# Performance work log

Hardware: AMD Instinct MI355X
Metric: run time of the kernel (lower is better)

## Reference

```python
import jax, jax.numpy as jnp
import numpy as np

DX, DY, MR, MBAR, NT, B, GOUT = 16, 8, 64, 256, 9, 4, 64
HX, EX, HRNN, HB = 1024, 512, 512, 2048
BB_IN = 1 + EX + HRNN


def setup_inputs() -> dict:
    key = jax.random.key(0)
    ks = jax.random.split(key, 12)
    total = (NT - 1) * MBAR + 1  # 2049 hidden-process time points
    X = jax.random.randint(ks[0], (B, total, DX), 0, 50).astype(jnp.float32)  # molecule counts
    Y = jax.random.normal(ks[1], (B, NT, DY), dtype=jnp.float32)
    # R: cumulative integrated reaction rates (non-decreasing in time)
    R = jnp.cumsum(jax.random.uniform(ks[2], (B, total, MR), dtype=jnp.float32) * 0.01, axis=1)
    stoich = (jax.random.randint(ks[3], (DX, MR), 0, 3) - 1).astype(jnp.float32)  # entries in {-1,0,1}
    times_t = jnp.linspace(0.0, 8.0, NT).astype(jnp.float32)
    times_tau = jnp.linspace(0.0, 1.0, MBAR).astype(jnp.float32)
    sc = lambda k, sh: jax.random.normal(k, sh, dtype=jnp.float32) * np.float32(1.0 / np.sqrt(sh[0]))
    Wx1, bx1 = sc(ks[4], (DX, HX)), jnp.zeros(HX, jnp.float32)
    Wx2, bx2 = sc(ks[5], (HX, EX)), jnp.zeros(EX, jnp.float32)
    Wih = sc(ks[6], (DY, HRNN))
    Whh = sc(ks[7], (HRNN, HRNN))
    bh = jnp.zeros(HRNN, jnp.float32)
    Wb1, bb1 = sc(ks[8], (BB_IN, HB)), jnp.zeros(HB, jnp.float32)
    Wb2, bb2 = sc(ks[9], (HB, GOUT)), jnp.zeros(GOUT, jnp.float32)
    return dict(X=X, Y=Y, R=R, stoich=stoich, times_t=times_t, times_tau=times_tau,
                Wx1=Wx1, bx1=bx1, Wx2=Wx2, bx2=bx2, Wih=Wih, Whh=Whh, bh=bh,
                Wb1=Wb1, bb1=bb1, Wb2=Wb2, bb2=bb2, k=1, k_prime=1, q=0, q_prime=1)


def reference(X, Y, R, stoich, times_t, times_tau,
              Wx1, bx1, Wx2, bx2, Wih, Whh, bh, Wb1, bb1, Wb2, bb2,
              k, k_prime, q, q_prime):
    """stochastic_integral_vectorized: gather displaced states, run the
    martingale network forward on base and displaced states, masked
    accumulation weighted by rate increments. Returns [GOUT]."""
    m_bar = times_tau.shape[0]
    base = k_prime * m_bar

    # --- Y encoder (Elman RNN over the observation slice, final hidden state) ---
    Yslice = Y[q, k + 1:, :]                       # [T_rem, DY]
    def rnn_step(h, y):
        return jnp.tanh(y @ Wih + h @ Whh + bh), None
    eY, _ = jax.lax.scan(rnn_step, jnp.zeros(Whh.shape[0], X.dtype), Yslice)  # [HRNN]

    # --- batched martingale forward: t [N], Xb [N, DX] -> [N, GOUT] ---
    def batched_forward(t, Xb):
        eX = jnp.tanh(Xb @ Wx1 + bx1) @ Wx2 + bx2          # [N, EX]
        eYb = jnp.broadcast_to(eY, (Xb.shape[0], eY.shape[0]))
        inp = jnp.concatenate([t[:, None], eX, eYb], axis=1)  # [N, 1+EX+HRNN]
        return jnp.tanh(inp @ Wb1 + bb1) @ Wb2 + bb2       # [N, GOUT]

    Xbase = X[q_prime, base:base + m_bar, :]               # [M_bar, DX]
    t = times_t[k] + times_tau                              # [M_bar]
    nn = batched_forward(t, Xbase)                          # [M_bar, GOUT]

    mr = stoich.shape[1]
    X_disp = Xbase[None, :, :] + stoich.T[:, None, :]       # [MR, M_bar, DX]
    valid = jnp.all(X_disp >= 0, axis=-1)                   # [MR, M_bar]
    nn_disp = batched_forward(jnp.tile(t, mr),
                              X_disp.reshape(mr * m_bar, -1)).reshape(mr, m_bar, -1)

    R_delta = R[q_prime, base + 1:base + m_bar + 1, :] - R[q_prime, base:base + m_bar, :]  # [M_bar, MR]
    si = jnp.einsum('jmg,mj,jm->g', nn_disp - nn[None], R_delta, valid.astype(nn.dtype))
    return si
```

## Files before the change

### kernel.cpp

```cpp
#include <hip/hip_runtime.h>
#include <math.h>

#define DXc   16
#define MRc   64
#define MBARc 256
#define NTc   9
#define DYc   8
#define HXc   1024
#define EXc   512
#define HRc   512
#define HBc   2048
#define GOUTc 64
#define TOTc  2049

using bf16x8 = __attribute__((ext_vector_type(8))) short;
using f32x4  = __attribute__((ext_vector_type(4))) float;

typedef unsigned int u32;
typedef u32 __attribute__((address_space(1))) gbl_u32;
typedef u32 __attribute__((address_space(3))) lds_u32;

__device__ __forceinline__ float fast_tanh(float x){
    float e = __expf(2.0f * x);
    return 1.0f - 2.0f / (e + 1.0f);
}

__device__ __forceinline__ short f2bf(float f){
    unsigned u = __builtin_bit_cast(unsigned, f);
    u = (u + 0x7FFFu + ((u >> 16) & 1u)) >> 16;
    return (short)u;
}

__device__ __forceinline__ void gld_lds16(const short* g, short* l){
    __builtin_amdgcn_global_load_lds((const gbl_u32*)g, (lds_u32*)l, 16, 0, 0);
}

__global__ void prep_kernel(const float* __restrict__ stoich, const float* __restrict__ Wx1,
                            const float* __restrict__ Wx2, const float* __restrict__ Wb1,
                            const float* __restrict__ X, const float* __restrict__ R,
                            const float* __restrict__ bx1, const float* __restrict__ bx2,
                            const int* kpptr, const int* qpptr,
                            float* __restrict__ SW, short* __restrict__ Wx2a,
                            short* __restrict__ Wb1p, float* __restrict__ XW,
                            float* __restrict__ T1, float* __restrict__ wrow,
                            float* __restrict__ hb0, float* __restrict__ dacc,
                            float* __restrict__ outz, float* __restrict__ eXb,
                            float* __restrict__ Z2Bacc){
    int b = blockIdx.x, tid = threadIdx.x;
    if (b < 256){
        int idx = b * 256 + tid;
        int j = idx >> 10, c = idx & 1023;
        float acc = 0.f;
        #pragma unroll
        for (int d = 0; d < DXc; ++d) acc += stoich[d * MRc + j] * Wx1[d * HXc + c];
        SW[idx] = acc;
    } else if (b < 512){
        size_t grp = (size_t)(b - 256) * 256 + tid;
        int lane = grp & 63;
        size_t t2 = grp >> 6;
        int kt = t2 & 15, mt = t2 >> 4;
        int c  = mt * 16 + (lane & 15);
        int e0 = kt * 32 + ((lane >> 4) << 3);
        short o8[8];
        #pragma unroll
        for (int jj = 0; jj < 8; ++jj) o8[jj] = f2bf(Wx2[(size_t)c * EXc + e0 + jj]);
        *(bf16x8*)(Wx2a + grp * 8) = *(bf16x8*)o8;
    } else if (b < 1024){
        size_t grp = (size_t)(b - 512) * 256 + tid;
        int lane = grp & 63;
        size_t t2 = grp >> 6;
        int kt = t2 & 15, nt = t2 >> 4;
        int n  = nt * 16 + (lane & 15);
        int k0 = kt * 32 + ((lane >> 4) << 3);
        short o8[8];
        #pragma unroll
        for (int jj = 0; jj < 8; ++jj) o8[jj] = f2bf(Wb1[(size_t)(1 + k0 + jj) * HBc + n]);
        *(bf16x8*)(Wb1p + grp * 8) = *(bf16x8*)o8;
    } else if (b < 2048){
        int idx = (b - 1024) * 256 + tid;
        int m = idx >> 10, c = idx & 1023;
        int base = kpptr[0] * MBARc;
        const float* xr = X + ((size_t)qpptr[0] * TOTc + base + m) * DXc;
        float acc = bx1[c];
        #pragma unroll
        for (int d = 0; d < DXc; ++d) acc += xr[d] * Wx1[d * HXc + c];
        XW[idx] = acc;
        T1[idx] = fast_tanh(acc);
    } else if (b < 2112){
        int j = b - 2048, m = tid;
        int base = kpptr[0] * MBARc;
        int qp = qpptr[0];
        const float* xr = X + ((size_t)qp * TOTc + base + m) * DXc;
        bool valid = true;
        #pragma unroll
        for (int d = 0; d < DXc; ++d) valid = valid && (xr[d] + stoich[d * MRc + j] >= 0.f);
        size_t rb = (size_t)qp * TOTc * MRc;
        float rd = R[rb + (size_t)(base + 1 + m) * MRc + j] - R[rb + (size_t)(base + m) * MRc + j];
        wrow[j * MBARc + m] = valid ? rd : 0.f;
    } else if (b == 2112){
        hb0[tid] = 0.f; hb0[tid + 256] = 0.f;
        #pragma unroll
        for (int l = 0; l < 8; ++l) dacc[tid + l * 256] = 0.f;
        if (tid < GOUTc) outz[tid] = 0.f;
    } else if (b < 2625){
        int idx = (b - 2113) * 256 + tid;
        eXb[idx] = bx2[idx & 511];
    } else {
        Z2Bacc[(size_t)(b - 2625) * 256 + tid] = 0.f;
    }
}

__global__ __launch_bounds__(512) void rnn_step_kernel(
    const float* __restrict__ Y, const float* __restrict__ Wih,
    const float* __restrict__ Whh, const float* __restrict__ bh,
    const int* kptr, const int* qptr,
    const float* __restrict__ h_cur, float* __restrict__ h_next, int step){
    __shared__ float hs[HRc];
    __shared__ float psum[8][64];
    int tid = threadIdx.x;
    int o   = tid & 63;
    int seg = tid >> 6;
    int out = blockIdx.x * 64 + o;
    int k = kptr[0], q = qptr[0];
    int t = k + 1 + step;
    hs[tid] = h_cur[tid];
    __syncthreads();
    if (t >= NTc){
        if (seg == 0) h_next[out] = hs[out];
        return;
    }
    int k0 = seg * 64;
    float a0 = 0.f, a1 = 0.f, a2 = 0.f, a3 = 0.f;
    #pragma unroll 4
    for (int kk = 0; kk < 64; kk += 4){
        a0 += hs[k0 + kk + 0] * Whh[(size_t)(k0 + kk + 0) * HRc + out];
        a1 += hs[k0 + kk + 1] * Whh[(size_t)(k0 + kk + 1) * HRc + out];
        a2 += hs[k0 + kk + 2] * Whh[(size_t)(k0 + kk + 2) * HRc + out];
        a3 += hs[k0 + kk + 3] * Whh[(size_t)(k0 + kk + 3) * HRc + out];
    }
    psum[seg][o] = (a0 + a1) + (a2 + a3);
    __syncthreads();
    if (seg == 0){
        float a = 0.f;
        #pragma unroll
        for (int r = 0; r < 8; ++r) a += psum[r][o];
        const float* y = Y + (q * NTc + t) * DYc;
        float z = bh[out];
        #pragma unroll
        for (int d = 0; d < DYc; ++d) z += y[d] * Wih[d * HRc + out];
        h_next[out] = fast_tanh(z + a);
    }
}

__global__ __launch_bounds__(256) void cy_kernel(const float* __restrict__ eY,
                                                 const float* __restrict__ Wb1,
                                                 const float* __restrict__ bb1,
                                                 float* __restrict__ cY){
    __shared__ float psum[4][64];
    int tid = threadIdx.x;
    int o = tid & 63, seg = tid >> 6;
    int h = blockIdx.x * 64 + o;
    int e0 = seg * 128;
    float acc = 0.f;
    #pragma unroll 4
    for (int e = 0; e < 128; ++e)
        acc += eY[e0 + e] * Wb1[(size_t)(1 + EXc + e0 + e) * HBc + h];
    psum[seg][o] = acc;
    __syncthreads();
    if (seg == 0)
        cY[h] = bb1[h] + psum[0][o] + psum[1][o] + psum[2][o] + psum[3][o];
}

__global__ __launch_bounds__(256) void exbase_kernel(const float* __restrict__ T1,
                                                     const float* __restrict__ Wx2,
                                                     float* __restrict__ eXb){
    __shared__ float t1s[8 * 128];
    int b = blockIdx.x, tid = threadIdx.x;
    int mg = b & 31, eh = (b >> 5) & 1, kq = b >> 6;
    int m0 = mg * 8, e = eh * 256 + tid, k0 = kq * 128;
    #pragma unroll
    for (int l = 0; l < 4; ++l){
        int idx = tid + l * 256;
        t1s[idx] = T1[(size_t)(m0 + (idx >> 7)) * HXc + k0 + (idx & 127)];
    }
    __syncthreads();
    float acc[8] = {};
    #pragma unroll 4
    for (int kk = 0; kk < 128; ++kk){
        float wv = Wx2[(size_t)(k0 + kk) * EXc + e];
        #pragma unroll
        for (int mm = 0; mm < 8; ++mm) acc[mm] += t1s[mm * 128 + kk] * wv;
    }
    #pragma unroll
    for (int mm = 0; mm < 8; ++mm)
        atomicAdd(&eXb[(size_t)(m0 + mm) * EXc + e], acc[mm]);
}

__global__ __launch_bounds__(256) void z2acc_kernel(const float* __restrict__ eXb,
                                                    const float* __restrict__ Wb1,
                                                    float* __restrict__ Z2Bacc){
    __shared__ float exs[8 * 256];
    int b = blockIdx.x, tid = threadIdx.x;
    int mg = b & 31, hh = (b >> 5) & 7, kq = b >> 8;
    int m0 = mg * 8, h = hh * 256 + tid, k0 = kq * 256;
    #pragma unroll
    for (int l = 0; l < 8; ++l){
        int idx = tid + l * 256;
        exs[idx] = eXb[(size_t)(m0 + (idx >> 8)) * EXc + k0 + (idx & 255)];
    }
    __syncthreads();
    float acc[8] = {};
    #pragma unroll 4
    for (int kk = 0; kk < 256; ++kk){
        float wv = Wb1[(size_t)(1 + k0 + kk) * HBc + h];
        #pragma unroll
        for (int mm = 0; mm < 8; ++mm) acc[mm] += exs[mm * 256 + kk] * wv;
    }
    #pragma unroll
    for (int mm = 0; mm < 8; ++mm)
        atomicAdd(&Z2Bacc[(size_t)(m0 + mm) * HBc + h], acc[mm]);
}

__global__ void tb_kernel(const float* __restrict__ Z2Bacc, const float* __restrict__ Wb1,
                          const float* __restrict__ cY, const float* __restrict__ times_t,
                          const float* __restrict__ times_tau, const int* kptr,
                          float* __restrict__ TB){
    int b = blockIdx.x, tid = threadIdx.x;
    int m = b >> 3, h = (b & 7) * 256 + tid;
    float tk = times_t[kptr[0]];
    size_t idx = (size_t)m * HBc + h;
    float z = Z2Bacc[idx] + (tk + times_tau[m]) * Wb1[h] + cY[h];
    TB[idx] = fast_tanh(z);
}

__global__ void act_delta_kernel(const float* __restrict__ XW, const float* __restrict__ T1,
                                 const float* __restrict__ SW, short* __restrict__ A1p){
    size_t grp = (size_t)blockIdx.x * 256 + threadIdx.x;
    int lane = grp & 63;
    size_t t2 = grp >> 6;
    int kt = t2 & 31;
    int mt = (int)(t2 >> 5);
    int m  = mt * 16 + (lane & 15);
    int c0 = kt * 32 + ((lane >> 4) << 3);
    int j    = m >> 8;
    int mloc = m & 255;
    const float* xwr = XW + (size_t)mloc * HXc + c0;
    const float* t1r = T1 + (size_t)mloc * HXc + c0;
    const float* swr = SW + (size_t)j * HXc + c0;
    short o8[8];
    #pragma unroll
    for (int i = 0; i < 8; ++i)
        o8[i] = f2bf(fast_tanh(xwr[i] + swr[i]) - t1r[i]);
    *(bf16x8*)(A1p + grp * 8) = *(bf16x8*)o8;
}

#define MMGRID(aa, bb) {                                                       \
    _Pragma("unroll") for (int i_ = 0; i_ < 4; ++i_)                           \
        _Pragma("unroll") for (int j_ = 0; j_ < 4; ++j_)                       \
            acc[i_][j_] = __builtin_amdgcn_mfma_f32_16x16x32_bf16(aa[i_], bb[j_], acc[i_][j_], 0, 0, 0); }

__device__ __forceinline__ void stage32(const short* __restrict__ Ap, const short* __restrict__ Bp,
                                        short* As, short* Bs,
                                        int at0, int bt0, int s, int KTOT, int wave, int lane){
    #pragma unroll
    for (int c = 0; c < 4; ++c){
        int ci = wave * 4 + c;
        int half = ci >> 3;
        int t    = ci & 7;
        const short* src = half ? (Bp + ((size_t)(bt0 + t) * KTOT + s) * 512 + lane * 8)
                                : (Ap + ((size_t)(at0 + t) * KTOT + s) * 512 + lane * 8);
        short* dst = (half ? Bs : As) + t * 512;
        gld_lds16(src, dst);
    }
}

#define STAGE_COMPUTE(As, Bs) {                                                       \
    bf16x8 af[4], bfr[4];                                                             \
    _Pragma("unroll") for (int i_ = 0; i_ < 4; ++i_)                                  \
        af[i_] = *(const bf16x8*)((As) + ((wm * 4 + i_) * 512) + lane * 8);           \
    _Pragma("unroll") for (int j_ = 0; j_ < 4; ++j_)                                  \
        bfr[j_] = *(const bf16x8*)((Bs) + ((wn * 4 + j_) * 512) + lane * 8);          \
    MMGRID(af, bfr); }

__global__ __launch_bounds__(256) void w12_mfma(
    const short* __restrict__ Ap, const short* __restrict__ Bp,
    short* __restrict__ W12p){
    const int KTOT = 16, S = 16;
    __shared__ __align__(16) short Asb[2][4096];
    __shared__ __align__(16) short Bsb[2][4096];
    int tid = threadIdx.x;
    int wave = tid >> 6, lane = tid & 63;
    int wm = wave >> 1, wn = wave & 1;
    int bx = blockIdx.x, by = blockIdx.y;
    int quad = lane >> 4, llo = lane & 15;
    f32x4 acc[4][4];
    #pragma unroll
    for (int i = 0; i < 4; ++i)
        #pragma unroll
        for (int j = 0; j < 4; ++j) acc[i][j] = (f32x4){0.f, 0.f, 0.f, 0.f};
    stage32(Ap, Bp, Asb[0], Bsb[0], by * 8, bx * 8, 0, KTOT, wave, lane);
    for (int s = 0; s < S; ++s){
        int buf = s & 1;
        __syncthreads();
        if (s + 1 < S)
            stage32(Ap, Bp, Asb[buf ^ 1], Bsb[buf ^ 1], by * 8, bx * 8, s + 1, KTOT, wave, lane);
        STAGE_COMPUTE(Asb[buf], Bsb[buf]);
    }
    #pragma unroll
    for (int j = 0; j < 4; ++j){
        int h = bx * 128 + wn * 64 + j * 16 + llo;
        #pragma unroll
        for (int i = 0; i < 4; ++i){
            #pragma unroll
            for (int r = 0; r < 4; ++r){
                int c = by * 128 + wm * 64 + i * 16 + quad * 4 + r;
                W12p[(((size_t)(h >> 4) * 32 + (c >> 5)) * 64 + ((c & 31) >> 3) * 16 + llo) * 8 + (c & 7)] =
                    f2bf(acc[i][j][r]);
            }
        }
    }
}

__device__ __forceinline__ void stage24(const short* __restrict__ Ap, const short* __restrict__ Bp,
                                        short* As, short* Bs,
                                        int at0, int bt0, int s, int wave, int lane){
    #pragma unroll
    for (int c = 0; c < 6; ++c){
        int ci = wave * 6 + c;
        const short* src;
        short* dst;
        if (ci < 8){
            src = Ap + ((size_t)(at0 + ci) * 32 + s) * 512 + lane * 8;
            dst = As + ci * 512;
        } else {
            int t = ci - 8;
            src = Bp + ((size_t)(bt0 + t) * 32 + s) * 512 + lane * 8;
            dst = Bs + t * 512;
        }
        gld_lds16(src, dst);
    }
}

__global__ __launch_bounds__(256, 2) void gemm_big(
    const short* __restrict__ Ap, const short* __restrict__ Bp,
    const float* __restrict__ TB, const float* __restrict__ wrow,
    float* __restrict__ dacc){
    const int S = 32;
    __shared__ __align__(16) short Asb[2][4096];
    __shared__ __align__(16) short Bsb[2][8192];
    int tid = threadIdx.x;
    int wave = tid >> 6, lane = tid & 63;
    int wm = wave >> 1, wn = wave & 1;
    int bm = blockIdx.x, bn = blockIdx.y;
    int quad = lane >> 4, llo = lane & 15;
    f32x4 acc[4][8];
    #pragma unroll
    for (int i = 0; i < 4; ++i)
        #pragma unroll
        for (int j = 0; j < 8; ++j) acc[i][j] = (f32x4){0.f, 0.f, 0.f, 0.f};
    stage24(Ap, Bp, Asb[0], Bsb[0], bm * 8, bn * 16, 0, wave, lane);
    for (int s = 0; s < S; ++s){
        int buf = s & 1;
        __syncthreads();
        if (s + 1 < S)
            stage24(Ap, Bp, Asb[buf ^ 1], Bsb[buf ^ 1], bm * 8, bn * 16, s + 1, wave, lane);
        {
            bf16x8 af[4], bfr[8];
            #pragma unroll
            for (int i = 0; i < 4; ++i)
                af[i] = *(const bf16x8*)(Asb[buf] + ((wm * 4 + i) * 512) + lane * 8);
            #pragma unroll
            for (int j = 0; j < 8; ++j)
                bfr[j] = *(const bf16x8*)(Bsb[buf] + ((wn * 8 + j) * 512) + lane * 8);
            #pragma unroll
            for (int i = 0; i < 4; ++i)
                #pragma unroll
                for (int j = 0; j < 8; ++j)
                    acc[i][j] = __builtin_amdgcn_mfma_f32_16x16x32_bf16(af[i], bfr[j], acc[i][j], 0, 0, 0);
        }
    }
    int nj[8];
    #pragma unroll
    for (int j = 0; j < 8; ++j) nj[j] = bn * 256 + wn * 128 + j * 16 + llo;
    float part[8] = {};
    #pragma unroll
    for (int i = 0; i < 4; ++i){
        #pragma unroll
        for (int r = 0; r < 4; ++r){
            int m = bm * 128 + wm * 64 + i * 16 + quad * 4 + r;
            float wr = wrow[m];
            const float* trow = TB + (size_t)(m & 255) * HBc;
            #pragma unroll
            for (int j = 0; j < 8; ++j){
                float tb  = trow[nj[j]];
                float tdz = fast_tanh(acc[i][j][r]);
                float num = tdz * (1.0f - tb * tb);
                float den = 1.0f + tb * tdz;
                part[j] += wr * num * __builtin_amdgcn_rcpf(den);
            }
        }
    }
    #pragma unroll
    for (int j = 0; j < 8; ++j){
        part[j] += __shfl_xor(part[j], 16);
        part[j] += __shfl_xor(part[j], 32);
    }
    __shared__ float redn[256];
    redn[tid] = 0.f;
    __syncthreads();
    if (lane < 16){
        #pragma unroll
        for (int j = 0; j < 8; ++j)
            atomicAdd(&redn[wn * 128 + j * 16 + llo], part[j]);
    }
    __syncthreads();
    atomicAdd(&dacc[bn * 256 + tid], redn[tid]);
}

__global__ void out_kernel(const float* __restrict__ dacc, const float* __restrict__ Wb2,
                           float* __restrict__ out){
    __shared__ float red[4][64];
    int tid = threadIdx.x;
    int g = tid & 63, seg = tid >> 6;
    int h0 = blockIdx.x * 256 + seg * 64;
    float s = 0.f;
    #pragma unroll 8
    for (int hh = 0; hh < 64; ++hh)
        s += dacc[h0 + hh] * Wb2[(size_t)(h0 + hh) * GOUTc + g];
    red[seg][g] = s;
    __syncthreads();
    if (tid < 64)
        atomicAdd(&out[tid], red[0][tid] + red[1][tid] + red[2][tid] + red[3][tid]);
}

extern "C" void kernel_launch(void* const* d_in, const int* in_sizes, int n_in,
                              void* d_out, int out_size, void* d_ws, size_t ws_size,
                              hipStream_t stream){
    const float* X         = (const float*)d_in[0];
    const float* Y         = (const float*)d_in[1];
    const float* R         = (const float*)d_in[2];
    const float* stoich    = (const float*)d_in[3];
    const float* times_t   = (const float*)d_in[4];
    const float* times_tau = (const float*)d_in[5];
    const float* Wx1 = (const float*)d_in[6];
    const float* bx1 = (const float*)d_in[7];
    const float* Wx2 = (const float*)d_in[8];
    const float* bx2 = (const float*)d_in[9];
    const float* Wih = (const float*)d_in[10];
    const float* Whh = (const float*)d_in[11];
    const float* bh  = (const float*)d_in[12];
    const float* Wb1 = (const float*)d_in[13];
    const float* bb1 = (const float*)d_in[14];
    const float* Wb2 = (const float*)d_in[15];
    const int* kp  = (const int*)d_in[17];
    const int* kpp = (const int*)d_in[18];
    const int* qp  = (const int*)d_in[19];
    const int* qpp = (const int*)d_in[20];
    float* out = (float*)d_out;

    float* ws     = (float*)d_ws;
    float* hb0    = ws;
    float* hb1    = ws + 512;
    float* cY     = ws + 1024;
    float* dacc   = ws + 3072;
    float* wrow   = ws + 5120;
    float* SW     = ws + 21504;
    float* XW     = ws + 87040;
    float* T1     = ws + 349184;
    float* eXb    = ws + 611328;
    float* TB     = ws + 742400;
    float* Z2Bacc = ws + 1266688;
    short* A1p    = (short*)(ws + 1790976);
    short* Wx2a   = (short*)(ws + 10179584);
    short* Wb1p   = (short*)(ws + 10441728);
    short* W12p   = (short*)(ws + 10966016);

    prep_kernel     <<<4673, 256, 0, stream>>>(stoich, Wx1, Wx2, Wb1, X, R, bx1, bx2, kpp, qpp,
                                               SW, Wx2a, Wb1p, XW, T1, wrow, hb0, dacc, out,
                                               eXb, Z2Bacc);
    w12_mfma        <<<dim3(16, 8), 256, 0, stream>>>(Wx2a, Wb1p, W12p);
    act_delta_kernel<<<8192, 256, 0, stream>>>(XW, T1, SW, A1p);
    for (int s = 0; s < 8; ++s){
        const float* hc = (s & 1) ? hb1 : hb0;
        float*       hn = (s & 1) ? hb0 : hb1;
        rnn_step_kernel<<<8, 512, 0, stream>>>(Y, Wih, Whh, bh, kp, qp, hc, hn, s);
    }
    cy_kernel       <<<32,   256, 0, stream>>>(hb0, Wb1, bb1, cY);
    exbase_kernel   <<<512,  256, 0, stream>>>(T1, Wx2, eXb);
    z2acc_kernel    <<<512,  256, 0, stream>>>(eXb, Wb1, Z2Bacc);
    tb_kernel       <<<2048, 256, 0, stream>>>(Z2Bacc, Wb1, cY, times_t, times_tau, kp, TB);
    gemm_big        <<<dim3(128, 8), 256, 0, stream>>>(A1p, W12p, TB, wrow, dacc);
    out_kernel      <<<8,    256, 0, stream>>>(dacc, Wb2, out);
}
```

Before: 295.4 us.

## Merge independent kernels and run RNN steps in one persistent grid-synced kernel

Folds the W12 MFMA GEMM, the activation-delta packing and the eX base GEMM into a single launch that dispatches on block index. The eight per-step RNN launches and the cY projection become one 8-block kernel that synchronises steps through a global atomic counter with acquire/release ordering. The aim is to cut the number of kernel launches and the launch gaps on the serial RNN chain. The spin barrier depends on all 8 blocks being resident at once and adds a polling cost on each step.

```diff
diff --git a/kernel.cpp b/kernel.cpp
--- a/kernel.cpp
+++ b/kernel.cpp
@@ -45,7 +45,7 @@
                             float* __restrict__ T1, float* __restrict__ wrow,
                             float* __restrict__ hb0, float* __restrict__ dacc,
                             float* __restrict__ outz, float* __restrict__ eXb,
-                            float* __restrict__ Z2Bacc){
+                            float* __restrict__ Z2Bacc, int* __restrict__ cnt){
     int b = blockIdx.x, tid = threadIdx.x;
     if (b < 256){
         int idx = b * 256 + tid;
@@ -102,6 +102,7 @@
         #pragma unroll
         for (int l = 0; l < 8; ++l) dacc[tid + l * 256] = 0.f;
         if (tid < GOUTc) outz[tid] = 0.f;
+        if (tid == 0) cnt[0] = 0;
     } else if (b < 2625){
         int idx = (b - 2113) * 256 + tid;
         eXb[idx] = bx2[idx & 511];
@@ -110,90 +111,198 @@
     }
 }
 
-__global__ __launch_bounds__(512) void rnn_step_kernel(
+#define MMGRID(aa, bb) {                                                       \
+    _Pragma("unroll") for (int i_ = 0; i_ < 4; ++i_)                           \
+        _Pragma("unroll") for (int j_ = 0; j_ < 4; ++j_)                       \
+            acc[i_][j_] = __builtin_amdgcn_mfma_f32_16x16x32_bf16(aa[i_], bb[j_], acc[i_][j_], 0, 0, 0); }
+
+__device__ __forceinline__ void stage32(const short* __restrict__ Ap, const short* __restrict__ Bp,
+                                        short* As, short* Bs,
+                                        int at0, int bt0, int s, int KTOT, int wave, int lane){
+    #pragma unroll
+    for (int c = 0; c < 4; ++c){
+        int ci = wave * 4 + c;
+        int half = ci >> 3;
+        int t    = ci & 7;
+        const short* src = half ? (Bp + ((size_t)(bt0 + t) * KTOT + s) * 512 + lane * 8)
+                                : (Ap + ((size_t)(at0 + t) * KTOT + s) * 512 + lane * 8);
+        short* dst = (half ? Bs : As) + t * 512;
+        gld_lds16(src, dst);
+    }
+}
+
+#define STAGE_COMPUTE(As, Bs) {                                                       \
+    bf16x8 af[4], bfr[4];                                                             \
+    _Pragma("unroll") for (int i_ = 0; i_ < 4; ++i_)                                  \
+        af[i_] = *(const bf16x8*)((As) + ((wm * 4 + i_) * 512) + lane * 8);           \
+    _Pragma("unroll") for (int j_ = 0; j_ < 4; ++j_)                                  \
+        bfr[j_] = *(const bf16x8*)((Bs) + ((wn * 4 + j_) * 512) + lane * 8);          \
+    MMGRID(af, bfr); }
+
+__global__ __launch_bounds__(256) void w12_act_ex_kernel(
+    const short* __restrict__ Wx2a, const short* __restrict__ Wb1p,
+    short* __restrict__ W12p,
+    const float* __restrict__ XW, const float* __restrict__ T1,
+    const float* __restrict__ SW, short* __restrict__ A1p,
+    const float* __restrict__ Wx2, float* __restrict__ eXb){
+    __shared__ __align__(16) short Asb[2][4096];
+    __shared__ __align__(16) short Bsb[2][4096];
+    int b = blockIdx.x, tid = threadIdx.x;
+    if (b < 128){
+        const int KTOT = 16, S = 16;
+        int wave = tid >> 6, lane = tid & 63;
+        int wm = wave >> 1, wn = wave & 1;
+        int bx = b & 15, by = b >> 4;
+        int quad = lane >> 4, llo = lane & 15;
+        f32x4 acc[4][4];
+        #pragma unroll
+        for (int i = 0; i < 4; ++i)
+            #pragma unroll
+            for (int j = 0; j < 4; ++j) acc[i][j] = (f32x4){0.f, 0.f, 0.f, 0.f};
+        stage32(Wx2a, Wb1p, Asb[0], Bsb[0], by * 8, bx * 8, 0, KTOT, wave, lane);
+        for (int s = 0; s < S; ++s){
+            int buf = s & 1;
+            __syncthreads();
+            if (s + 1 < S)
+                stage32(Wx2a, Wb1p, Asb[buf ^ 1], Bsb[buf ^ 1], by * 8, bx * 8, s + 1, KTOT, wave, lane);
+            STAGE_COMPUTE(Asb[buf], Bsb[buf]);
+        }
+        #pragma unroll
+        for (int j = 0; j < 4; ++j){
+            int h = bx * 128 + wn * 64 + j * 16 + llo;
+            #pragma unroll
+            for (int i = 0; i < 4; ++i){
+                #pragma unroll
+                for (int r = 0; r < 4; ++r){
+                    int c = by * 128 + wm * 64 + i * 16 + quad * 4 + r;
+                    W12p[(((size_t)(h >> 4) * 32 + (c >> 5)) * 64 + ((c & 31) >> 3) * 16 + llo) * 8 + (c & 7)] =
+                        f2bf(acc[i][j][r]);
+                }
+            }
+        }
+    } else if (b < 8320){
+        size_t grp = (size_t)(b - 128) * 256 + tid;
+        int lane = grp & 63;
+        size_t t2 = grp >> 6;
+        int kt = t2 & 31;
+        int mt = (int)(t2 >> 5);
+        int m  = mt * 16 + (lane & 15);
+        int c0 = kt * 32 + ((lane >> 4) << 3);
+        int j    = m >> 8;
+        int mloc = m & 255;
+        const float* xwr = XW + (size_t)mloc * HXc + c0;
+        const float* t1r = T1 + (size_t)mloc * HXc + c0;
+        const float* swr = SW + (size_t)j * HXc + c0;
+        short o8[8];
+        #pragma unroll
+        for (int i = 0; i < 8; ++i)
+            o8[i] = f2bf(fast_tanh(xwr[i] + swr[i]) - t1r[i]);
+        *(bf16x8*)(A1p + grp * 8) = *(bf16x8*)o8;
+    } else {
+        __shared__ float t1s[8 * 128];
+        int bb = b - 8320;
+        int mg = bb & 31, eh = (bb >> 5) & 1, kq = bb >> 6;
+        int m0 = mg * 8, e = eh * 256 + tid, k0 = kq * 128;
+        #pragma unroll
+        for (int l = 0; l < 4; ++l){
+            int idx = tid + l * 256;
+            t1s[idx] = T1[(size_t)(m0 + (idx >> 7)) * HXc + k0 + (idx & 127)];
+        }
+        __syncthreads();
+        float acc[8] = {};
+        #pragma unroll 4
+        for (int kk = 0; kk < 128; ++kk){
+            float wv = Wx2[(size_t)(k0 + kk) * EXc + e];
+            #pragma unroll
+            for (int mm = 0; mm < 8; ++mm) acc[mm] += t1s[mm * 128 + kk] * wv;
+        }
+        #pragma unroll
+        for (int mm = 0; mm < 8; ++mm)
+            atomicAdd(&eXb[(size_t)(m0 + mm) * EXc + e], acc[mm]);
+    }
+}
+
+__global__ __launch_bounds__(512) void rnn_cy_kernel(
     const float* __restrict__ Y, const float* __restrict__ Wih,
     const float* __restrict__ Whh, const float* __restrict__ bh,
+    const float* __restrict__ Wb1, const float* __restrict__ bb1,
     const int* kptr, const int* qptr,
-    const float* __restrict__ h_cur, float* __restrict__ h_next, int step){
+    float* __restrict__ hb0, float* __restrict__ hb1,
+    int* __restrict__ cnt, float* __restrict__ cY){
     __shared__ float hs[HRc];
     __shared__ float psum[8][64];
-    int tid = threadIdx.x;
-    int o   = tid & 63;
-    int seg = tid >> 6;
-    int out = blockIdx.x * 64 + o;
-    int k = kptr[0], q = qptr[0];
-    int t = k + 1 + step;
-    hs[tid] = h_cur[tid];
-    __syncthreads();
-    if (t >= NTc){
-        if (seg == 0) h_next[out] = hs[out];
-        return;
-    }
-    int k0 = seg * 64;
-    float a0 = 0.f, a1 = 0.f, a2 = 0.f, a3 = 0.f;
-    #pragma unroll 4
-    for (int kk = 0; kk < 64; kk += 4){
-        a0 += hs[k0 + kk + 0] * Whh[(size_t)(k0 + kk + 0) * HRc + out];
-        a1 += hs[k0 + kk + 1] * Whh[(size_t)(k0 + kk + 1) * HRc + out];
-        a2 += hs[k0 + kk + 2] * Whh[(size_t)(k0 + kk + 2) * HRc + out];
-        a3 += hs[k0 + kk + 3] * Whh[(size_t)(k0 + kk + 3) * HRc + out];
-    }
-    psum[seg][o] = (a0 + a1) + (a2 + a3);
-    __syncthreads();
-    if (seg == 0){
-        float a = 0.f;
-        #pragma unroll
-        for (int r = 0; r < 8; ++r) a += psum[r][o];
-        const float* y = Y + (q * NTc + t) * DYc;
-        float z = bh[out];
-        #pragma unroll
-        for (int d = 0; d < DYc; ++d) z += y[d] * Wih[d * HRc + out];
-        h_next[out] = fast_tanh(z + a);
-    }
-}
-
-__global__ __launch_bounds__(256) void cy_kernel(const float* __restrict__ eY,
-                                                 const float* __restrict__ Wb1,
-                                                 const float* __restrict__ bb1,
-                                                 float* __restrict__ cY){
-    __shared__ float psum[4][64];
+    __shared__ float ps2[2][256];
     int tid = threadIdx.x;
     int o = tid & 63, seg = tid >> 6;
-    int h = blockIdx.x * 64 + o;
-    int e0 = seg * 128;
+    int b = blockIdx.x;
+    int out = b * 64 + o;
+    int k = kptr[0], q = qptr[0];
+    hs[tid] = 0.f;
+    __syncthreads();
+    for (int s = 0; s < 8; ++s){
+        float* dst = (s & 1) ? hb0 : hb1;
+        if (s > 0){
+            const float* src = (s & 1) ? hb1 : hb0;
+            if (tid == 0){
+                int guard = 0;
+                while (__hip_atomic_load(cnt, __ATOMIC_ACQUIRE, __HIP_MEMORY_SCOPE_AGENT) < 8 * s
+                       && ++guard < (1 << 26)) {}
+            }
+            __syncthreads();
+            hs[tid] = __hip_atomic_load(src + tid, __ATOMIC_RELAXED, __HIP_MEMORY_SCOPE_AGENT);
+            __syncthreads();
+        }
+        int t = k + 1 + s;
+        if (t < NTc){
+            int k0 = seg * 64;
+            float a0 = 0.f, a1 = 0.f, a2 = 0.f, a3 = 0.f;
+            #pragma unroll 4
+            for (int kk = 0; kk < 64; kk += 4){
+                a0 += hs[k0 + kk + 0] * Whh[(size_t)(k0 + kk + 0) * HRc + out];
+                a1 += hs[k0 + kk + 1] * Whh[(size_t)(k0 + kk + 1) * HRc + out];
+                a2 += hs[k0 + kk + 2] * Whh[(size_t)(k0 + kk + 2) * HRc + out];
+                a3 += hs[k0 + kk + 3] * Whh[(size_t)(k0 + kk + 3) * HRc + out];
+            }
+            psum[seg][o] = (a0 + a1) + (a2 + a3);
+            __syncthreads();
+            if (seg == 0){
+                float a = 0.f;
+                #pragma unroll
+                for (int r = 0; r < 8; ++r) a += psum[r][o];
+                const float* y = Y + (q * NTc + t) * DYc;
+                float z = bh[out];
+                #pragma unroll
+                for (int d = 0; d < DYc; ++d) z += y[d] * Wih[d * HRc + out];
+                __hip_atomic_store(dst + out, fast_tanh(z + a), __ATOMIC_RELEASE, __HIP_MEMORY_SCOPE_AGENT);
+            }
+            __syncthreads();
+        } else {
+            if (seg == 0)
+                __hip_atomic_store(dst + out, hs[out], __ATOMIC_RELEASE, __HIP_MEMORY_SCOPE_AGENT);
+            __syncthreads();
+        }
+        if (tid == 0)
+            __hip_atomic_fetch_add(cnt, 1, __ATOMIC_RELEASE, __HIP_MEMORY_SCOPE_AGENT);
+    }
+    if (tid == 0){
+        int guard = 0;
+        while (__hip_atomic_load(cnt, __ATOMIC_ACQUIRE, __HIP_MEMORY_SCOPE_AGENT) < 64
+               && ++guard < (1 << 26)) {}
+    }
+    __syncthreads();
+    hs[tid] = __hip_atomic_load(hb0 + tid, __ATOMIC_RELAXED, __HIP_MEMORY_SCOPE_AGENT);
+    __syncthreads();
+    int o2 = tid & 255, sg = tid >> 8;
+    int h = b * 256 + o2;
     float acc = 0.f;
+    int e0 = sg * 256;
     #pragma unroll 4
-    for (int e = 0; e < 128; ++e)
-        acc += eY[e0 + e] * Wb1[(size_t)(1 + EXc + e0 + e) * HBc + h];
-    psum[seg][o] = acc;
-    __syncthreads();
-    if (seg == 0)
-        cY[h] = bb1[h] + psum[0][o] + psum[1][o] + psum[2][o] + psum[3][o];
-}
-
-__global__ __launch_bounds__(256) void exbase_kernel(const float* __restrict__ T1,
-                                                     const float* __restrict__ Wx2,
-                                                     float* __restrict__ eXb){
-    __shared__ float t1s[8 * 128];
-    int b = blockIdx.x, tid = threadIdx.x;
-    int mg = b & 31, eh = (b >> 5) & 1, kq = b >> 6;
-    int m0 = mg * 8, e = eh * 256 + tid, k0 = kq * 128;
-    #pragma unroll
-    for (int l = 0; l < 4; ++l){
-        int idx = tid + l * 256;
-        t1s[idx] = T1[(size_t)(m0 + (idx >> 7)) * HXc + k0 + (idx & 127)];
-    }
-    __syncthreads();
-    float acc[8] = {};
-    #pragma unroll 4
-    for (int kk = 0; kk < 128; ++kk){
-        float wv = Wx2[(size_t)(k0 + kk) * EXc + e];
-        #pragma unroll
-        for (int mm = 0; mm < 8; ++mm) acc[mm] += t1s[mm * 128 + kk] * wv;
-    }
-    #pragma unroll
-    for (int mm = 0; mm < 8; ++mm)
-        atomicAdd(&eXb[(size_t)(m0 + mm) * EXc + e], acc[mm]);
+    for (int e = 0; e < 256; ++e)
+        acc += hs[e0 + e] * Wb1[(size_t)(1 + EXc + e0 + e) * HBc + h];
+    ps2[sg][o2] = acc;
+    __syncthreads();
+    if (sg == 0)
+        cY[h] = bb1[h] + ps2[0][o2] + ps2[1][o2];
 }
 
 __global__ __launch_bounds__(256) void z2acc_kernel(const float* __restrict__ eXb,
@@ -231,94 +340,6 @@
     size_t idx = (size_t)m * HBc + h;
     float z = Z2Bacc[idx] + (tk + times_tau[m]) * Wb1[h] + cY[h];
     TB[idx] = fast_tanh(z);
-}
-
-__global__ void act_delta_kernel(const float* __restrict__ XW, const float* __restrict__ T1,
-                                 const float* __restrict__ SW, short* __restrict__ A1p){
-    size_t grp = (size_t)blockIdx.x * 256 + threadIdx.x;
-    int lane = grp & 63;
-    size_t t2 = grp >> 6;
-    int kt = t2 & 31;
-    int mt = (int)(t2 >> 5);
-    int m  = mt * 16 + (lane & 15);
-    int c0 = kt * 32 + ((lane >> 4) << 3);
-    int j    = m >> 8;
-    int mloc = m & 255;
-    const float* xwr = XW + (size_t)mloc * HXc + c0;
-    const float* t1r = T1 + (size_t)mloc * HXc + c0;
-    const float* swr = SW + (size_t)j * HXc + c0;
-    short o8[8];
-    #pragma unroll
-    for (int i = 0; i < 8; ++i)
-        o8[i] = f2bf(fast_tanh(xwr[i] + swr[i]) - t1r[i]);
-    *(bf16x8*)(A1p + grp * 8) = *(bf16x8*)o8;
-}
-
-#define MMGRID(aa, bb) {                                                       \
-    _Pragma("unroll") for (int i_ = 0; i_ < 4; ++i_)                           \
-        _Pragma("unroll") for (int j_ = 0; j_ < 4; ++j_)                       \
-            acc[i_][j_] = __builtin_amdgcn_mfma_f32_16x16x32_bf16(aa[i_], bb[j_], acc[i_][j_], 0, 0, 0); }
-
-__device__ __forceinline__ void stage32(const short* __restrict__ Ap, const short* __restrict__ Bp,
-                                        short* As, short* Bs,
-                                        int at0, int bt0, int s, int KTOT, int wave, int lane){
-    #pragma unroll
-    for (int c = 0; c < 4; ++c){
-        int ci = wave * 4 + c;
-        int half = ci >> 3;
-        int t    = ci & 7;
-        const short* src = half ? (Bp + ((size_t)(bt0 + t) * KTOT + s) * 512 + lane * 8)
-                                : (Ap + ((size_t)(at0 + t) * KTOT + s) * 512 + lane * 8);
-        short* dst = (half ? Bs : As) + t * 512;
-        gld_lds16(src, dst);
-    }
-}
-
-#define STAGE_COMPUTE(As, Bs) {                                                       \
-    bf16x8 af[4], bfr[4];                                                             \
-    _Pragma("unroll") for (int i_ = 0; i_ < 4; ++i_)                                  \
-        af[i_] = *(const bf16x8*)((As) + ((wm * 4 + i_) * 512) + lane * 8);           \
-    _Pragma("unroll") for (int j_ = 0; j_ < 4; ++j_)                                  \
-        bfr[j_] = *(const bf16x8*)((Bs) + ((wn * 4 + j_) * 512) + lane * 8);          \
-    MMGRID(af, bfr); }
-
-__global__ __launch_bounds__(256) void w12_mfma(
-    const short* __restrict__ Ap, const short* __restrict__ Bp,
-    short* __restrict__ W12p){
-    const int KTOT = 16, S = 16;
-    __shared__ __align__(16) short Asb[2][4096];
-    __shared__ __align__(16) short Bsb[2][4096];
-    int tid = threadIdx.x;
-    int wave = tid >> 6, lane = tid & 63;
-    int wm = wave >> 1, wn = wave & 1;
-    int bx = blockIdx.x, by = blockIdx.y;
-    int quad = lane >> 4, llo = lane & 15;
-    f32x4 acc[4][4];
-    #pragma unroll
-    for (int i = 0; i < 4; ++i)
-        #pragma unroll
-        for (int j = 0; j < 4; ++j) acc[i][j] = (f32x4){0.f, 0.f, 0.f, 0.f};
-    stage32(Ap, Bp, Asb[0], Bsb[0], by * 8, bx * 8, 0, KTOT, wave, lane);
-    for (int s = 0; s < S; ++s){
-        int buf = s & 1;
-        __syncthreads();
-        if (s + 1 < S)
-            stage32(Ap, Bp, Asb[buf ^ 1], Bsb[buf ^ 1], by * 8, bx * 8, s + 1, KTOT, wave, lane);
-        STAGE_COMPUTE(Asb[buf], Bsb[buf]);
-    }
-    #pragma unroll
-    for (int j = 0; j < 4; ++j){
-        int h = bx * 128 + wn * 64 + j * 16 + llo;
-        #pragma unroll
-        for (int i = 0; i < 4; ++i){
-            #pragma unroll
-            for (int r = 0; r < 4; ++r){
-                int c = by * 128 + wm * 64 + i * 16 + quad * 4 + r;
-                W12p[(((size_t)(h >> 4) * 32 + (c >> 5)) * 64 + ((c & 31) >> 3) * 16 + llo) * 8 + (c & 7)] =
-                    f2bf(acc[i][j][r]);
-            }
-        }
-    }
 }
 
 __device__ __forceinline__ void stage24(const short* __restrict__ Ap, const short* __restrict__ Bp,
@@ -474,21 +495,15 @@
     short* Wx2a   = (short*)(ws + 10179584);
     short* Wb1p   = (short*)(ws + 10441728);
     short* W12p   = (short*)(ws + 10966016);
-
-    prep_kernel     <<<4673, 256, 0, stream>>>(stoich, Wx1, Wx2, Wb1, X, R, bx1, bx2, kpp, qpp,
-                                               SW, Wx2a, Wb1p, XW, T1, wrow, hb0, dacc, out,
-                                               eXb, Z2Bacc);
-    w12_mfma        <<<dim3(16, 8), 256, 0, stream>>>(Wx2a, Wb1p, W12p);
-    act_delta_kernel<<<8192, 256, 0, stream>>>(XW, T1, SW, A1p);
-    for (int s = 0; s < 8; ++s){
-        const float* hc = (s & 1) ? hb1 : hb0;
-        float*       hn = (s & 1) ? hb0 : hb1;
-        rnn_step_kernel<<<8, 512, 0, stream>>>(Y, Wih, Whh, bh, kp, qp, hc, hn, s);
-    }
-    cy_kernel       <<<32,   256, 0, stream>>>(hb0, Wb1, bb1, cY);
-    exbase_kernel   <<<512,  256, 0, stream>>>(T1, Wx2, eXb);
-    z2acc_kernel    <<<512,  256, 0, stream>>>(eXb, Wb1, Z2Bacc);
-    tb_kernel       <<<2048, 256, 0, stream>>>(Z2Bacc, Wb1, cY, times_t, times_tau, kp, TB);
-    gemm_big        <<<dim3(128, 8), 256, 0, stream>>>(A1p, W12p, TB, wrow, dacc);
-    out_kernel      <<<8,    256, 0, stream>>>(dacc, Wb2, out);
-}
+    int*   cnt    = (int*)(ws + 12014592);
+
+    prep_kernel      <<<4673, 256, 0, stream>>>(stoich, Wx1, Wx2, Wb1, X, R, bx1, bx2, kpp, qpp,
+                                                SW, Wx2a, Wb1p, XW, T1, wrow, hb0, dacc, out,
+                                                eXb, Z2Bacc, cnt);
+    w12_act_ex_kernel<<<8832, 256, 0, stream>>>(Wx2a, Wb1p, W12p, XW, T1, SW, A1p, Wx2, eXb);
+    rnn_cy_kernel    <<<8,    512, 0, stream>>>(Y, Wih, Whh, bh, Wb1, bb1, kp, qp, hb0, hb1, cnt, cY);
+    z2acc_kernel     <<<512,  256, 0, stream>>>(eXb, Wb1, Z2Bacc);
+    tb_kernel        <<<2048, 256, 0, stream>>>(Z2Bacc, Wb1, cY, times_t, times_tau, kp, TB);
+    gemm_big         <<<dim3(128, 8), 256, 0, stream>>>(A1p, W12p, TB, wrow, dacc);
+    out_kernel       <<<8,    256, 0, stream>>>(dacc, Wb2, out);
+}
```

Result: no change. 293.5 us (-0.6%).
